# Kernel optimization log

Hardware: AMD Instinct MI355X
Metric: run time of the kernel (lower is better)

## Reference

```python
import jax, jax.numpy as jnp
import numpy as np

N_NODES = 50000
N_EDGES = 600000
C = 128
T = 2          # layer index t
NU = 1         # DRew nu parameter
EPS = 0.0      # GIN eps


def mlp(x, W1, b1, W2, b2):
    # instantiate_mlp with final_activation=False, batch_norm=False:
    # Linear -> ReLU -> Linear
    return jax.nn.relu(x @ W1 + b1) @ W2 + b2


def setup_inputs() -> dict:
    key = jax.random.key(0)
    ks = jax.random.split(key, 16)
    node_embeddings = jax.random.normal(ks[0], (T + 1, N_NODES, C), dtype=jnp.float32)
    edge_index = jax.random.randint(ks[1], (2, N_EDGES), 0, N_NODES, dtype=jnp.int32)
    edge_weights = jax.random.randint(ks[2], (N_EDGES,), 1, T + 2, dtype=jnp.int32)  # hops 1..3
    s = 1.0 / np.sqrt(C)
    def lin(k):
        kw, kb = jax.random.split(k)
        return (jax.random.uniform(kw, (C, C), jnp.float32, -s, s),
                jax.random.uniform(kb, (C,), jnp.float32, -s, s))
    loop_W1, loop_b1 = lin(ks[3]); loop_W2, loop_b2 = lin(ks[4])
    rel_W1, rel_b1 = lin(ks[5]); rel_W2, rel_b2 = lin(ks[6])
    # T higher-hop MLPs (k = 2 .. T+1), stacked along axis 0
    hh1 = [lin(k) for k in jax.random.split(ks[7], T)]
    hh2 = [lin(k) for k in jax.random.split(ks[8], T)]
    hh_W1 = jnp.stack([w for w, _ in hh1]); hh_b1 = jnp.stack([b for _, b in hh1])
    hh_W2 = jnp.stack([w for w, _ in hh2]); hh_b2 = jnp.stack([b for _, b in hh2])
    hop_coef = jax.random.normal(ks[9], (T + 1,), dtype=jnp.float32)
    return dict(t=T, node_embeddings=node_embeddings, edge_index=edge_index,
                edge_weights=edge_weights,
                loop_W1=loop_W1, loop_b1=loop_b1, loop_W2=loop_W2, loop_b2=loop_b2,
                rel_W1=rel_W1, rel_b1=rel_b1, rel_W2=rel_W2, rel_b2=rel_b2,
                hh_W1=hh_W1, hh_b1=hh_b1, hh_W2=hh_W2, hh_b2=hh_b2,
                hop_coef=hop_coef)


def reference(t, node_embeddings, edge_index, edge_weights,
              loop_W1, loop_b1, loop_W2, loop_b2,
              rel_W1, rel_b1, rel_W2, rel_b2,
              hh_W1, hh_b1, hh_W2, hh_b2, hop_coef):
    x_t = node_embeddings[t]                       # [N, C]
    n = x_t.shape[0]
    row, col = edge_index[0], edge_index[1]        # sparse A: out[row] += X[col]
    dt = x_t.dtype

    hops = []
    # hop 1: relational MLP on current-layer embeddings
    h1 = mlp(x_t, rel_W1, rel_b1, rel_W2, rel_b2)
    m1 = (edge_weights == 1).astype(dt)[:, None]
    hops.append(jax.ops.segment_sum(h1[col] * m1, row, num_segments=n))
    # hops k = 2 .. t+1: per-hop MLP on delayed embeddings (DRew)
    for k in range(2, t + 2):
        delay = max(0, k - NU)
        hk = mlp(node_embeddings[t - delay],
                 hh_W1[k - 2], hh_b1[k - 2], hh_W2[k - 2], hh_b2[k - 2])
        mk = (edge_weights == k).astype(dt)[:, None]
        hops.append(jax.ops.segment_sum(hk[col] * mk, row, num_segments=n))

    by_hop = jnp.stack(hops)                       # [t+1, N, C]
    self_term = mlp((1.0 + EPS) * x_t, loop_W1, loop_b1, loop_W2, loop_b2)
    return self_term + jnp.einsum('k,knc->nc', hop_coef, by_hop)
```

## Files before the change

kernel.cpp:

```cpp
#include <hip/hip_runtime.h>

#define N_NODES 50000
#define N_EDGES 600000
#define C 128
#define STRIPS 3125
#define N_TASKS 4
#define MLP_BLOCKS 256
#define SLOT_STRIDE 512

typedef __bf16 bf16;
typedef __attribute__((ext_vector_type(8))) __bf16 bf16x8;
typedef __attribute__((ext_vector_type(4))) __bf16 bf16x4;
typedef __attribute__((ext_vector_type(2))) __bf16 bf16x2;
typedef __attribute__((ext_vector_type(4))) float f32x4;
typedef __attribute__((ext_vector_type(2))) float f32x2;

struct PtrsV { const void* p[8]; };

__device__ __forceinline__ int bf16_wild(unsigned short w) {
    int exp = (w >> 7) & 0xFF;
    int mant = w & 0x7F;
    if (exp == 0xFF) return 1;
    if (exp >= 133) return 1;
    if (exp == 0) return mant != 0 ? 1 : 0;
    if (exp <= 114) return 1;
    return 0;
}

__global__ void __launch_bounds__(256) detect_zero_kernel(
    const unsigned short* __restrict__ emb,
    const unsigned short* __restrict__ w,
    const unsigned short* __restrict__ b,
    const unsigned short* __restrict__ hc,
    int* __restrict__ flags, int* __restrict__ deg)
{
    if (blockIdx.x == 0) {
        int lane = threadIdx.x;
        if (lane >= 64) return;
        int ce = 0, cw = 0, cb = 0, ch = 0;
        for (int j = 0; j < 4; ++j) {
            ce += bf16_wild(emb[lane * 4 + j]);
            cw += bf16_wild(w[lane * 4 + j]);
        }
        for (int j = 0; j < 2; ++j) cb += bf16_wild(b[lane * 2 + j]);
        if (lane < 3) ch = bf16_wild(hc[lane]);
        for (int off = 32; off > 0; off >>= 1) {
            ce += __shfl_down(ce, off);
            cw += __shfl_down(cw, off);
            cb += __shfl_down(cb, off);
            ch += __shfl_down(ch, off);
        }
        if (lane == 0) {
            int wf = (cw >= 16) ? 1 : 0;
            flags[0] = (ce >= 16) ? 1 : 0;
            flags[1] = wf;
            flags[2] = (cb >= 8) ? 1 : 0;
            flags[3] = (ch > 0) ? 1 : wf;
        }
    } else {
        int i = (blockIdx.x - 1) * 256 + threadIdx.x;
        if (i < N_NODES) deg[i] = 0;
    }
}

__global__ void __launch_bounds__(256) pack_kernel(
    PtrsV wmats, PtrsV bvecs, const void* hc_raw,
    const int* __restrict__ flags,
    bf16* __restrict__ pw, float* __restrict__ cbias, float* __restrict__ ccoef)
{
    int tid = blockIdx.x * 256 + threadIdx.x;
    int wf = flags[1], bfl = flags[2], hf = flags[3];
    if (tid < 8 * 16384) {
        int m    = tid >> 14;
        int r    = tid & 16383;
        int j    = r & 7;
        int lane = (r >> 3) & 63;
        int n0   = (r >> 9) & 7;
        int kk   = r >> 12;
        int k = kk * 32 + (lane >> 4) * 8 + j;
        int n = n0 * 16 + (lane & 15);
        int idx = k * C + n + ((m == 4 || m == 5) ? 16384 : 0);
        float v = wf ? ((const float*)wmats.p[m])[idx]
                     : (float)((const bf16*)wmats.p[m])[idx];
        pw[tid] = (bf16)v;
    } else if (tid < 8 * 16384 + 1024) {
        int j = tid - 8 * 16384;
        int m = j >> 7, n = j & 127;
        int idx = n + ((m == 4 || m == 5) ? 128 : 0);
        float v = bfl ? ((const float*)bvecs.p[m])[idx]
                      : (float)((const bf16*)bvecs.p[m])[idx];
        cbias[j] = v;
    } else if (tid < 8 * 16384 + 1024 + 3) {
        int i = tid - (8 * 16384 + 1024);
        float v = hf ? ((const float*)hc_raw)[i]
                     : (float)((const bf16*)hc_raw)[i];
        ccoef[i] = v;
    }
}

__global__ __launch_bounds__(512, 2) void mlp_kernel(
    const void* __restrict__ emb_raw,
    const bf16* __restrict__ pw,
    const float* __restrict__ cbias,
    const float* __restrict__ ccoef,
    const int* __restrict__ flags,
    bf16* __restrict__ h,
    bf16* __restrict__ hs)
{
    __shared__ bf16 sW[32768];
    __shared__ bf16 sH[8][16][136];
    const int tid  = threadIdx.x;
    const int wave = tid >> 6, lane = tid & 63;
    const int task  = blockIdx.x & 3;
    const int bslot = blockIdx.x >> 2;
    const int lrow = lane & 15, lquad = lane >> 4;
    bf16 (*sh)[136] = sH[wave];

    const int m1_of[4] = {0, 2, 4, 6};
    const int ly_of[4] = {2, 1, 0, 2};
    const int m1 = m1_of[task];
    const float oscale = (task == 0) ? ccoef[0] : (task == 1) ? ccoef[1]
                       : (task == 2) ? ccoef[2] : 1.0f;
    bf16* outp = (task == 3) ? hs : (h + (size_t)task * N_NODES * C);
    const int emb_f32 = flags[0];
    const size_t lbase = (size_t)ly_of[task] * N_NODES * C;

    {
        const f32x4* src = (const f32x4*)(pw + (size_t)m1 * 16384);
        f32x4* dst = (f32x4*)sW;
        #pragma unroll
        for (int i = 0; i < 8; ++i)
            dst[i * 512 + tid] = src[i * 512 + tid];
    }
    __syncthreads();
    const bf16x8* w1v = (const bf16x8*)sW;
    const bf16x8* w2v = w1v + 2048;

    float b1f[8], b2f[8];
    #pragma unroll
    for (int n0 = 0; n0 < 8; ++n0) {
        b1f[n0] = cbias[m1 * 128 + n0 * 16 + lrow];
        b2f[n0] = cbias[(m1 + 1) * 128 + n0 * 16 + lrow];
    }

    int s = bslot * 8 + wave;
    f32x4 u[8]; bf16x8 araw[4];

    {
        size_t xb = lbase + (size_t)(s * 16 + lrow) * C + lquad * 8;
        if (emb_f32) {
            const float* xf = (const float*)emb_raw + xb;
            #pragma unroll
            for (int kk = 0; kk < 4; ++kk) {
                u[kk * 2]     = *(const f32x4*)(xf + kk * 32);
                u[kk * 2 + 1] = *(const f32x4*)(xf + kk * 32 + 4);
            }
        } else {
            const bf16* x16 = (const bf16*)emb_raw + xb;
            #pragma unroll
            for (int kk = 0; kk < 4; ++kk)
                araw[kk] = *(const bf16x8*)(x16 + kk * 32);
        }
    }

    while (s < STRIPS) {
        const int snext = s + SLOT_STRIDE;

        bf16x8 af[4];
        if (emb_f32) {
            #pragma unroll
            for (int kk = 0; kk < 4; ++kk) {
                f32x4 u0 = u[kk * 2], u1 = u[kk * 2 + 1];
                bf16x8 v;
                v[0]=(bf16)u0[0]; v[1]=(bf16)u0[1]; v[2]=(bf16)u0[2]; v[3]=(bf16)u0[3];
                v[4]=(bf16)u1[0]; v[5]=(bf16)u1[1]; v[6]=(bf16)u1[2]; v[7]=(bf16)u1[3];
                af[kk] = v;
            }
        } else {
            #pragma unroll
            for (int kk = 0; kk < 4; ++kk) af[kk] = araw[kk];
        }

        if (snext < STRIPS) {
            size_t xb = lbase + (size_t)(snext * 16 + lrow) * C + lquad * 8;
            if (emb_f32) {
                const float* xf = (const float*)emb_raw + xb;
                #pragma unroll
                for (int kk = 0; kk < 4; ++kk) {
                    u[kk * 2]     = *(const f32x4*)(xf + kk * 32);
                    u[kk * 2 + 1] = *(const f32x4*)(xf + kk * 32 + 4);
                }
            } else {
                const bf16* x16 = (const bf16*)emb_raw + xb;
                #pragma unroll
                for (int kk = 0; kk < 4; ++kk)
                    araw[kk] = *(const bf16x8*)(x16 + kk * 32);
            }
        }

        #pragma unroll
        for (int n0 = 0; n0 < 8; ++n0) {
            bf16x8 bv0 = w1v[0 * 512 + n0 * 64 + lane];
            bf16x8 bv1 = w1v[1 * 512 + n0 * 64 + lane];
            bf16x8 bv2 = w1v[2 * 512 + n0 * 64 + lane];
            bf16x8 bv3 = w1v[3 * 512 + n0 * 64 + lane];
            int n = n0 * 16 + lrow;
            float bias = b1f[n0];
            f32x4 a4 = {0.f, 0.f, 0.f, 0.f};
            a4 = __builtin_amdgcn_mfma_f32_16x16x32_bf16(af[0], bv0, a4, 0, 0, 0);
            a4 = __builtin_amdgcn_mfma_f32_16x16x32_bf16(af[1], bv1, a4, 0, 0, 0);
            a4 = __builtin_amdgcn_mfma_f32_16x16x32_bf16(af[2], bv2, a4, 0, 0, 0);
            a4 = __builtin_amdgcn_mfma_f32_16x16x32_bf16(af[3], bv3, a4, 0, 0, 0);
            #pragma unroll
            for (int r = 0; r < 4; ++r) {
                float v = a4[r] + bias;
                v = v > 0.f ? v : 0.f;
                sh[lquad * 4 + r][n] = (bf16)v;
            }
        }

        bf16x8 ah[4];
        #pragma unroll
        for (int kk = 0; kk < 4; ++kk)
            ah[kk] = *(const bf16x8*)(&sh[lrow][kk * 32 + lquad * 8]);

        #pragma unroll
        for (int n0 = 0; n0 < 8; ++n0) {
            bf16x8 bv0 = w2v[0 * 512 + n0 * 64 + lane];
            bf16x8 bv1 = w2v[1 * 512 + n0 * 64 + lane];
            bf16x8 bv2 = w2v[2 * 512 + n0 * 64 + lane];
            bf16x8 bv3 = w2v[3 * 512 + n0 * 64 + lane];
            int n = n0 * 16 + lrow;
            float bias = b2f[n0];
            f32x4 a4 = {0.f, 0.f, 0.f, 0.f};
            a4 = __builtin_amdgcn_mfma_f32_16x16x32_bf16(ah[0], bv0, a4, 0, 0, 0);
            a4 = __builtin_amdgcn_mfma_f32_16x16x32_bf16(ah[1], bv1, a4, 0, 0, 0);
            a4 = __builtin_amdgcn_mfma_f32_16x16x32_bf16(ah[2], bv2, a4, 0, 0, 0);
            a4 = __builtin_amdgcn_mfma_f32_16x16x32_bf16(ah[3], bv3, a4, 0, 0, 0);
            #pragma unroll
            for (int r = 0; r < 4; ++r)
                sh[lquad * 4 + r][n] = (bf16)((a4[r] + bias) * oscale);
        }

        {
            int row = lane >> 2;
            int cs  = (lane & 3) * 32;
            bf16* dst = outp + (size_t)(s * 16) * C;
            #pragma unroll
            for (int j = 0; j < 4; ++j) {
                bf16x8 v = *(const bf16x8*)(&sh[row][cs + j * 8]);
                *(bf16x8*)(dst + (size_t)row * C + cs + j * 8) = v;
            }
        }

        s = snext;
    }
}

__global__ void __launch_bounds__(256) hist_kernel(
    const int* __restrict__ erow, int* __restrict__ deg)
{
    int e = blockIdx.x * 256 + threadIdx.x;
    if (e >= N_EDGES) return;
    atomicAdd(&deg[erow[e]], 1);
}

__device__ __forceinline__ int wave_incl_scan(int v, int lane) {
    int x = v;
    #pragma unroll
    for (int d = 1; d < 64; d <<= 1) {
        int t = __shfl_up(x, d);
        if (lane >= d) x += t;
    }
    return x;
}

__global__ void __launch_bounds__(256) scanA_kernel(
    const int* __restrict__ deg, int* __restrict__ offsets, int* __restrict__ btot)
{
    __shared__ int swave[4];
    int b = blockIdx.x, tid = threadIdx.x;
    int i = b * 256 + tid;
    int lane = tid & 63, wv = tid >> 6;
    int v = (i < N_NODES) ? deg[i] : 0;
    int x = wave_incl_scan(v, lane);
    if (lane == 63) swave[wv] = x;
    __syncthreads();
    int w0 = swave[0], w1 = swave[1], w2 = swave[2], w3 = swave[3];
    int wp = (wv > 0 ? w0 : 0) + (wv > 1 ? w1 : 0) + (wv > 2 ? w2 : 0);
    if (i < N_NODES) offsets[i] = wp + x - v;
    if (tid == 0) btot[b] = w0 + w1 + w2 + w3;
}

__global__ void __launch_bounds__(256) scanB_kernel(
    const int* __restrict__ btot, int* __restrict__ bbase, int nblk)
{
    __shared__ int swave[4];
    int tid = threadIdx.x;
    int lane = tid & 63, wv = tid >> 6;
    int v = (tid < nblk) ? btot[tid] : 0;
    int x = wave_incl_scan(v, lane);
    if (lane == 63) swave[wv] = x;
    __syncthreads();
    int w0 = swave[0], w1 = swave[1], w2 = swave[2], w3 = swave[3];
    int wp = (wv > 0 ? w0 : 0) + (wv > 1 ? w1 : 0) + (wv > 2 ? w2 : 0);
    if (tid < nblk) bbase[tid] = wp + x - v;
}

__global__ void __launch_bounds__(256) scanC_kernel(
    const int* __restrict__ bbase, int* __restrict__ offsets, int* __restrict__ cursor)
{
    int i = blockIdx.x * 256 + threadIdx.x;
    if (i < N_NODES) {
        int o = offsets[i] + bbase[blockIdx.x];
        offsets[i] = o;
        cursor[i] = o;
    }
    if (i == 0) offsets[N_NODES] = N_EDGES;
}

__global__ void __launch_bounds__(256) fill_kernel(
    const int* __restrict__ erow, const int* __restrict__ ecol,
    const int* __restrict__ ew,
    int* __restrict__ cursor, int* __restrict__ edata)
{
    int e = blockIdx.x * 256 + threadIdx.x;
    if (e >= N_EDGES) return;
    int dst = erow[e];
    int pos = atomicAdd(&cursor[dst], 1);
    edata[pos] = (ecol[e] << 2) | (ew[e] - 1);
}

__global__ void __launch_bounds__(256) gather_kernel(
    const int* __restrict__ offsets, const int* __restrict__ edata,
    const bf16* __restrict__ h,
    const bf16* __restrict__ hs,
    void* __restrict__ out,
    const int* __restrict__ flags)
{
    const int node = blockIdx.x * 4 + (threadIdx.x >> 6);
    if (node >= N_NODES) return;
    const int lane = threadIdx.x & 63;
    const int c = lane * 2;

    bf16x2 sv = *(const bf16x2*)(hs + (size_t)node * C + c);
    float a0 = (float)sv[0], a1 = (float)sv[1];

    const int s = offsets[node], e = offsets[node + 1];
    for (int base = s; base < e; base += 64) {
        int idx = base + lane;
        int ed_i = (idx < e) ? edata[idx] : 0;
        int cnt = e - base; if (cnt > 64) cnt = 64;
        int j = 0;
        for (; j + 8 <= cnt; j += 8) {
            float t0 = 0.f, t1 = 0.f;
            #pragma unroll
            for (int u = 0; u < 8; ++u) {
                int ed = __shfl(ed_i, j + u);
                bf16x2 v = *(const bf16x2*)(h + (size_t)(ed & 3) * (N_NODES * C)
                                              + (size_t)(ed >> 2) * C + c);
                t0 += (float)v[0];
                t1 += (float)v[1];
            }
            a0 += t0; a1 += t1;
        }
        for (; j + 4 <= cnt; j += 4) {
            int e0 = __shfl(ed_i, j);
            int e1 = __shfl(ed_i, j + 1);
            int e2 = __shfl(ed_i, j + 2);
            int e3 = __shfl(ed_i, j + 3);
            bf16x2 v0 = *(const bf16x2*)(h + (size_t)(e0 & 3) * (N_NODES * C) + (size_t)(e0 >> 2) * C + c);
            bf16x2 v1 = *(const bf16x2*)(h + (size_t)(e1 & 3) * (N_NODES * C) + (size_t)(e1 >> 2) * C + c);
            bf16x2 v2 = *(const bf16x2*)(h + (size_t)(e2 & 3) * (N_NODES * C) + (size_t)(e2 >> 2) * C + c);
            bf16x2 v3 = *(const bf16x2*)(h + (size_t)(e3 & 3) * (N_NODES * C) + (size_t)(e3 >> 2) * C + c);
            a0 += (float)v0[0] + (float)v1[0] + (float)v2[0] + (float)v3[0];
            a1 += (float)v0[1] + (float)v1[1] + (float)v2[1] + (float)v3[1];
        }
        for (; j < cnt; ++j) {
            int ed = __shfl(ed_i, j);
            bf16x2 v = *(const bf16x2*)(h + (size_t)(ed & 3) * (N_NODES * C) + (size_t)(ed >> 2) * C + c);
            a0 += (float)v[0];
            a1 += (float)v[1];
        }
    }

    if (flags[0]) {
        f32x2 o; o[0] = a0; o[1] = a1;
        *(f32x2*)((float*)out + (size_t)node * C + c) = o;
    } else {
        bf16x2 o; o[0] = (bf16)a0; o[1] = (bf16)a1;
        *(bf16x2*)((bf16*)out + (size_t)node * C + c) = o;
    }
}

extern "C" void kernel_launch(void* const* d_in, const int* in_sizes, int n_in,
                              void* d_out, int out_size, void* d_ws, size_t ws_size,
                              hipStream_t stream) {
    const void* emb = d_in[1];
    const int*  ei  = (const int*)d_in[2];
    const int*  ew  = (const int*)d_in[3];

    const size_t H_BYTES  = (size_t)3 * N_NODES * C * sizeof(bf16);
    const size_t HS_BYTES = (size_t)N_NODES * C * sizeof(bf16);
    const size_t PW_BYTES = (size_t)8 * 16384 * sizeof(bf16);
    bf16*  h      = (bf16*)d_ws;
    bf16*  hs     = (bf16*)((char*)d_ws + H_BYTES);
    bf16*  pw     = (bf16*)((char*)d_ws + H_BYTES + HS_BYTES);
    float* cbias  = (float*)((char*)d_ws + H_BYTES + HS_BYTES + PW_BYTES);
    float* ccoef  = cbias + 1024;
    int*   flags  = (int*)(ccoef + 4);
    int*   deg    = flags + 16;
    int*   cursor = deg + N_NODES;
    int*   offsets= cursor + N_NODES;
    int*   btot   = offsets + N_NODES + 8;
    int*   bbase  = btot + 256;
    int*   edata  = bbase + 256;

    PtrsV wptr;
    wptr.p[0] = d_in[8];   wptr.p[1] = d_in[10];
    wptr.p[2] = d_in[12];  wptr.p[3] = d_in[14];
    wptr.p[4] = d_in[12];  wptr.p[5] = d_in[14];
    wptr.p[6] = d_in[4];   wptr.p[7] = d_in[6];
    PtrsV bptr;
    bptr.p[0] = d_in[9];   bptr.p[1] = d_in[11];
    bptr.p[2] = d_in[13];  bptr.p[3] = d_in[15];
    bptr.p[4] = d_in[13];  bptr.p[5] = d_in[15];
    bptr.p[6] = d_in[5];   bptr.p[7] = d_in[7];

    const int NBLK = (N_NODES + 255) / 256;

    detect_zero_kernel<<<1 + NBLK, 256, 0, stream>>>(
        (const unsigned short*)emb, (const unsigned short*)d_in[8],
        (const unsigned short*)d_in[9], (const unsigned short*)d_in[16],
        flags, deg);

    pack_kernel<<<517, 256, 0, stream>>>(wptr, bptr, d_in[16], flags, pw, cbias, ccoef);

    const int* erow = ei;
    const int* ecol = ei + N_EDGES;
    hist_kernel<<<(N_EDGES + 255) / 256, 256, 0, stream>>>(erow, deg);
    scanA_kernel<<<NBLK, 256, 0, stream>>>(deg, offsets, btot);
    scanB_kernel<<<1, 256, 0, stream>>>(btot, bbase, NBLK);
    scanC_kernel<<<NBLK, 256, 0, stream>>>(bbase, offsets, cursor);
    fill_kernel<<<(N_EDGES + 255) / 256, 256, 0, stream>>>(erow, ecol, ew, cursor, edata);

    mlp_kernel<<<MLP_BLOCKS, 512, 0, stream>>>(
        emb, pw, cbias, ccoef, flags, h, hs);

    gather_kernel<<<(N_NODES + 3) / 4, 256, 0, stream>>>(
        offsets, edata, h, hs, d_out, flags);
}
```

Measured before the change: 269.4 us.

## Replace CSR build with fixed-capacity per-node edge buckets plus overflow pass

Swaps the histogram, three-pass scan and fill pipeline for a single bucketing kernel. It writes each edge into a fixed-capacity slot array per destination node, sized from the available workspace (at most 96 slots). Edges beyond a node's capacity go to an overflow list, which a small extra kernel adds into the output with atomics. This removes four launches and the scan dependency chain. In exchange it uses more memory, reads sparser bucket rows, and depends on enough workspace; otherwise it falls back to the CSR path.

```diff
diff --git a/kernel.cpp b/kernel.cpp
--- a/kernel.cpp
+++ b/kernel.cpp
@@ -6,7 +6,7 @@
 #define STRIPS 3125
 #define N_TASKS 4
 #define MLP_BLOCKS 256
-#define SLOT_STRIDE 512
+#define MAXOVF 16384
 
 typedef __bf16 bf16;
 typedef __attribute__((ext_vector_type(8))) __bf16 bf16x8;
@@ -32,7 +32,9 @@
     const unsigned short* __restrict__ w,
     const unsigned short* __restrict__ b,
     const unsigned short* __restrict__ hc,
-    int* __restrict__ flags, int* __restrict__ deg)
+    int* __restrict__ flags,
+    int* __restrict__ z0, int* __restrict__ z1,
+    int* __restrict__ ovf_cnt)
 {
     if (blockIdx.x == 0) {
         int lane = threadIdx.x;
@@ -59,7 +61,8 @@
         }
     } else {
         int i = (blockIdx.x - 1) * 256 + threadIdx.x;
-        if (i < N_NODES) deg[i] = 0;
+        if (i < N_NODES) { z0[i] = 0; z1[i] = 0; }
+        if (blockIdx.x == 1 && threadIdx.x == 0) *ovf_cnt = 0;
     }
 }
 
@@ -164,7 +167,7 @@
     }
 
     while (s < STRIPS) {
-        const int snext = s + SLOT_STRIDE;
+        const int snext = s + 512;
 
         bf16x8 af[4];
         if (emb_f32) {
@@ -257,6 +260,25 @@
     }
 }
 
+__global__ void __launch_bounds__(256) bucket_kernel(
+    const int* __restrict__ erow, const int* __restrict__ ecol,
+    const int* __restrict__ ew,
+    int* __restrict__ cursor, int* __restrict__ edata,
+    int* __restrict__ ovf_cnt, int* __restrict__ ovf, int cap)
+{
+    int e = blockIdx.x * 256 + threadIdx.x;
+    if (e >= N_EDGES) return;
+    int dst = erow[e];
+    int val = (ecol[e] << 2) | (ew[e] - 1);
+    int pos = atomicAdd(&cursor[dst], 1);
+    if (pos < cap) {
+        edata[(size_t)dst * cap + pos] = val;
+    } else {
+        int o = atomicAdd(ovf_cnt, 1);
+        if (o < MAXOVF) { ovf[2 * o] = dst; ovf[2 * o + 1] = val; }
+    }
+}
+
 __global__ void __launch_bounds__(256) hist_kernel(
     const int* __restrict__ erow, int* __restrict__ deg)
 {
@@ -332,11 +354,12 @@
 }
 
 __global__ void __launch_bounds__(256) gather_kernel(
-    const int* __restrict__ offsets, const int* __restrict__ edata,
+    const int* __restrict__ offsets, const int* __restrict__ cursor,
+    const int* __restrict__ edata,
     const bf16* __restrict__ h,
     const bf16* __restrict__ hs,
     void* __restrict__ out,
-    const int* __restrict__ flags)
+    const int* __restrict__ flags, int cap)
 {
     const int node = blockIdx.x * 4 + (threadIdx.x >> 6);
     if (node >= N_NODES) return;
@@ -346,10 +369,21 @@
     bf16x2 sv = *(const bf16x2*)(hs + (size_t)node * C + c);
     float a0 = (float)sv[0], a1 = (float)sv[1];
 
-    const int s = offsets[node], e = offsets[node + 1];
+    int s, e;
+    const int* ebase;
+    if (cap) {
+        int d = cursor[node];
+        if (d > cap) d = cap;
+        s = 0; e = d;
+        ebase = edata + (size_t)node * cap;
+    } else {
+        s = offsets[node]; e = offsets[node + 1];
+        ebase = edata;
+    }
+
     for (int base = s; base < e; base += 64) {
         int idx = base + lane;
-        int ed_i = (idx < e) ? edata[idx] : 0;
+        int ed_i = (idx < e) ? ebase[idx] : 0;
         int cnt = e - base; if (cnt > 64) cnt = 64;
         int j = 0;
         for (; j + 8 <= cnt; j += 8) {
@@ -393,6 +427,48 @@
     }
 }
 
+__device__ __forceinline__ float bf2f(unsigned short s) {
+    unsigned int u = (unsigned int)s << 16;
+    float f; __builtin_memcpy(&f, &u, 4); return f;
+}
+__device__ __forceinline__ unsigned short f2bf(float f) {
+    bf16 b = (bf16)f;
+    unsigned short s; __builtin_memcpy(&s, &b, 2); return s;
+}
+
+__global__ void __launch_bounds__(256) ovf_kernel(
+    const int* __restrict__ ovf_cnt, const int* __restrict__ ovf,
+    const bf16* __restrict__ h, void* __restrict__ out,
+    const int* __restrict__ flags)
+{
+    int n = *ovf_cnt; if (n > MAXOVF) n = MAXOVF;
+    if (n <= 0) return;
+    const int gw = (blockIdx.x * 256 + threadIdx.x) >> 6;
+    const int lane = threadIdx.x & 63;
+    const int nw = gridDim.x * 4;
+    const int c = lane * 2;
+    for (int i = gw; i < n; i += nw) {
+        int dst = ovf[2 * i], val = ovf[2 * i + 1];
+        bf16x2 v = *(const bf16x2*)(h + (size_t)(val & 3) * (N_NODES * C)
+                                      + (size_t)(val >> 2) * C + c);
+        float v0 = (float)v[0], v1 = (float)v[1];
+        if (flags[0]) {
+            atomicAdd((float*)out + (size_t)dst * C + c, v0);
+            atomicAdd((float*)out + (size_t)dst * C + c + 1, v1);
+        } else {
+            unsigned int* p = (unsigned int*)((bf16*)out + (size_t)dst * C + c);
+            unsigned int old = *p, assumed;
+            do {
+                assumed = old;
+                unsigned short lo = assumed & 0xFFFF, hi = assumed >> 16;
+                unsigned int nb = (unsigned int)f2bf(bf2f(lo) + v0)
+                                | ((unsigned int)f2bf(bf2f(hi) + v1) << 16);
+                old = atomicCAS(p, assumed, nb);
+            } while (old != assumed);
+        }
+    }
+}
+
 extern "C" void kernel_launch(void* const* d_in, const int* in_sizes, int n_in,
                               void* d_out, int out_size, void* d_ws, size_t ws_size,
                               hipStream_t stream) {
@@ -400,21 +476,28 @@
     const int*  ei  = (const int*)d_in[2];
     const int*  ew  = (const int*)d_in[3];
 
-    const size_t H_BYTES  = (size_t)3 * N_NODES * C * sizeof(bf16);
-    const size_t HS_BYTES = (size_t)N_NODES * C * sizeof(bf16);
-    const size_t PW_BYTES = (size_t)8 * 16384 * sizeof(bf16);
-    bf16*  h      = (bf16*)d_ws;
-    bf16*  hs     = (bf16*)((char*)d_ws + H_BYTES);
-    bf16*  pw     = (bf16*)((char*)d_ws + H_BYTES + HS_BYTES);
-    float* cbias  = (float*)((char*)d_ws + H_BYTES + HS_BYTES + PW_BYTES);
-    float* ccoef  = cbias + 1024;
-    int*   flags  = (int*)(ccoef + 4);
-    int*   deg    = flags + 16;
-    int*   cursor = deg + N_NODES;
-    int*   offsets= cursor + N_NODES;
-    int*   btot   = offsets + N_NODES + 8;
-    int*   bbase  = btot + 256;
-    int*   edata  = bbase + 256;
+    char* base = (char*)d_ws;
+    bf16*  h      = (bf16*)base;
+    bf16*  hs     = (bf16*)(base + 38400000);
+    bf16*  pw     = (bf16*)(base + 51200000);
+    float* cbias  = (float*)(base + 51462144);
+    float* ccoef  = (float*)(base + 51466240);
+    int*   flags  = (int*)(base + 51466256);
+    int*   ovf_cnt= (int*)(base + 51466288);
+    int*   cursor = (int*)(base + 51466752);
+
+    int*   ovf    = (int*)(base + 51666752);
+    int*   bedata = (int*)(base + 51797824);
+    size_t avail  = ws_size > 51797824 ? ws_size - 51797824 : 0;
+    int cap = (int)(avail / (4ull * N_NODES));
+    if (cap > 96) cap = 96;
+    cap &= ~15;
+
+    int*   deg    = (int*)(base + 51666752);
+    int*   offsets= (int*)(base + 51866752);
+    int*   btot   = (int*)(base + 52066816);
+    int*   bbase  = (int*)(base + 52067840);
+    int*   cedata = (int*)(base + 52068864);
 
     PtrsV wptr;
     wptr.p[0] = d_in[8];   wptr.p[1] = d_in[10];
@@ -428,25 +511,44 @@
     bptr.p[6] = d_in[5];   bptr.p[7] = d_in[7];
 
     const int NBLK = (N_NODES + 255) / 256;
-
-    detect_zero_kernel<<<1 + NBLK, 256, 0, stream>>>(
-        (const unsigned short*)emb, (const unsigned short*)d_in[8],
-        (const unsigned short*)d_in[9], (const unsigned short*)d_in[16],
-        flags, deg);
-
-    pack_kernel<<<517, 256, 0, stream>>>(wptr, bptr, d_in[16], flags, pw, cbias, ccoef);
-
+    const int EBLK = (N_EDGES + 255) / 256;
     const int* erow = ei;
     const int* ecol = ei + N_EDGES;
-    hist_kernel<<<(N_EDGES + 255) / 256, 256, 0, stream>>>(erow, deg);
-    scanA_kernel<<<NBLK, 256, 0, stream>>>(deg, offsets, btot);
-    scanB_kernel<<<1, 256, 0, stream>>>(btot, bbase, NBLK);
-    scanC_kernel<<<NBLK, 256, 0, stream>>>(bbase, offsets, cursor);
-    fill_kernel<<<(N_EDGES + 255) / 256, 256, 0, stream>>>(erow, ecol, ew, cursor, edata);
-
-    mlp_kernel<<<MLP_BLOCKS, 512, 0, stream>>>(
-        emb, pw, cbias, ccoef, flags, h, hs);
-
-    gather_kernel<<<(N_NODES + 3) / 4, 256, 0, stream>>>(
-        offsets, edata, h, hs, d_out, flags);
-}
+
+    if (cap >= 32) {
+        detect_zero_kernel<<<1 + NBLK, 256, 0, stream>>>(
+            (const unsigned short*)emb, (const unsigned short*)d_in[8],
+            (const unsigned short*)d_in[9], (const unsigned short*)d_in[16],
+            flags, cursor, cursor, ovf_cnt);
+
+        pack_kernel<<<517, 256, 0, stream>>>(wptr, bptr, d_in[16], flags, pw, cbias, ccoef);
+
+        bucket_kernel<<<EBLK, 256, 0, stream>>>(erow, ecol, ew, cursor, bedata,
+                                                ovf_cnt, ovf, cap);
+
+        mlp_kernel<<<MLP_BLOCKS, 512, 0, stream>>>(emb, pw, cbias, ccoef, flags, h, hs);
+
+        gather_kernel<<<(N_NODES + 3) / 4, 256, 0, stream>>>(
+            cursor, cursor, bedata, h, hs, d_out, flags, cap);
+
+        ovf_kernel<<<32, 256, 0, stream>>>(ovf_cnt, ovf, h, d_out, flags);
+    } else {
+        detect_zero_kernel<<<1 + NBLK, 256, 0, stream>>>(
+            (const unsigned short*)emb, (const unsigned short*)d_in[8],
+            (const unsigned short*)d_in[9], (const unsigned short*)d_in[16],
+            flags, deg, deg, ovf_cnt);
+
+        pack_kernel<<<517, 256, 0, stream>>>(wptr, bptr, d_in[16], flags, pw, cbias, ccoef);
+
+        hist_kernel<<<EBLK, 256, 0, stream>>>(erow, deg);
+        scanA_kernel<<<NBLK, 256, 0, stream>>>(deg, offsets, btot);
+        scanB_kernel<<<1, 256, 0, stream>>>(btot, bbase, NBLK);
+        scanC_kernel<<<NBLK, 256, 0, stream>>>(bbase, offsets, cursor);
+        fill_kernel<<<EBLK, 256, 0, stream>>>(erow, ecol, ew, cursor, cedata);
+
+        mlp_kernel<<<MLP_BLOCKS, 512, 0, stream>>>(emb, pw, cbias, ccoef, flags, h, hs);
+
+        gather_kernel<<<(N_NODES + 3) / 4, 256, 0, stream>>>(
+            offsets, cursor, cedata, h, hs, d_out, flags, 0);
+    }
+}
```

Result: faster. 244.9 us (-9.1%).
